# Performance work log

Measured on AMD Instinct MI355X. Metric: run time of the kernel, lower is better.

## Reference

```python
import jax, jax.numpy as jnp
import numpy as np
import math

B = 1024      # graphs
N = 64        # nodes per graph (padded, masked by node_mask)
BN = B * N    # total nodes
EPG = 192     # directed edges per graph
E = B * EPG


def setup_inputs() -> dict:
    key = jax.random.key(0)
    ks = jax.random.split(key, 40)

    def nrm(k, shp, s=0.02):
        return (jax.random.normal(k, shp) * s).astype(jnp.float32)

    mol_batch_x = jax.random.normal(ks[0], (BN, 19), dtype=jnp.float32)
    offs = jnp.arange(B, dtype=jnp.int32) * N
    src = jax.random.randint(ks[1], (B, EPG), 0, N, dtype=jnp.int32) + offs[:, None]
    dst = jax.random.randint(ks[2], (B, EPG), 0, N, dtype=jnp.int32) + offs[:, None]
    mol_batch_edge_index = jnp.stack([src.reshape(-1), dst.reshape(-1)], axis=0)
    mol_batch_batch = jnp.repeat(jnp.arange(B, dtype=jnp.int32), N)
    text_features = jax.random.normal(ks[3], (B, 300), dtype=jnp.float32)
    timesteps = jax.random.uniform(ks[4], (B,), minval=0.0, maxval=1000.0, dtype=jnp.float32)
    node_mask = (jax.random.uniform(ks[5], (B, N)) > 0.1).astype(jnp.float32)

    p = {
        'W_tr': nrm(ks[6], (19, 300)),   'b_tr': jnp.zeros((300,), jnp.float32),
        'W_c1': nrm(ks[7], (300, 600)),  'b_c1': jnp.zeros((600,), jnp.float32),
        'W_c2': nrm(ks[8], (600, 600)),  'b_c2': jnp.zeros((600,), jnp.float32),
        'W_c3': nrm(ks[9], (600, 600)),  'b_c3': jnp.zeros((600,), jnp.float32),
        'W_h1': nrm(ks[10], (600, 600)), 'b_h1': jnp.zeros((600,), jnp.float32),
        'W_h2': nrm(ks[11], (600, 600)), 'b_h2': jnp.zeros((600,), jnp.float32),
        'W_h3': nrm(ks[12], (600, 300)), 'b_h3': jnp.zeros((300,), jnp.float32),
        'ln_g': jnp.ones((300,), jnp.float32), 'ln_b': jnp.zeros((300,), jnp.float32),
        'W_t1': nrm(ks[13], (128, 512)), 'b_t1': jnp.zeros((512,), jnp.float32),
        'W_t2': nrm(ks[14], (512, 512)), 'b_t2': jnp.zeros((512,), jnp.float32),
        'W_e':  nrm(ks[15], (512, 3000)), 'b_e': jnp.zeros((3000,), jnp.float32),
    }
    return dict(mol_batch_x=mol_batch_x, mol_batch_edge_index=mol_batch_edge_index,
                mol_batch_batch=mol_batch_batch, text_features=text_features,
                timesteps=timesteps, node_mask=node_mask, **p)


def timestep_embedding(t, dim=128, max_period=10000.0):
    half = dim // 2
    freqs = jnp.exp(-math.log(max_period) * jnp.arange(half, dtype=jnp.float32) / half)
    args = t[:, None] * freqs[None]                 # [B, half]
    return jnp.concatenate([jnp.cos(args), jnp.sin(args)], axis=-1)  # [B, dim]


def gcn_conv(x, W, b, src, dst, num_nodes):
    # PyG GCNConv: D^{-1/2} (A + I) D^{-1/2} X W + b, edge weights 1
    h = x @ W                                             # [BN, F]
    deg = jnp.zeros((num_nodes,), h.dtype).at[dst].add(1.0) + 1.0  # in-degree + self-loop
    inv_sqrt = jax.lax.rsqrt(deg)
    coef = inv_sqrt[src] * inv_sqrt[dst]                  # [E]
    agg = jax.ops.segment_sum(h[src] * coef[:, None], dst, num_segments=num_nodes)
    return agg + h * (1.0 / deg)[:, None] + b             # self-loop norm = 1/deg


def global_mean_pool(x, batch, num_graphs):
    sums = jax.ops.segment_sum(x, batch, num_segments=num_graphs)
    cnts = jax.ops.segment_sum(jnp.ones((x.shape[0],), x.dtype), batch, num_segments=num_graphs)
    return sums / jnp.maximum(cnts, 1.0)[:, None]


def layer_norm(x, g, b, eps=1e-5):
    mu = jnp.mean(x, axis=-1, keepdims=True)
    var = jnp.mean(jnp.square(x - mu), axis=-1, keepdims=True)
    return (x - mu) * jax.lax.rsqrt(var + eps) * g + b


def reference(mol_batch_x, mol_batch_edge_index, mol_batch_batch, text_features,
              timesteps, node_mask, W_tr, b_tr, W_c1, b_c1, W_c2, b_c2, W_c3, b_c3,
              W_h1, b_h1, W_h2, b_h2, W_h3, b_h3, ln_g, ln_b,
              W_t1, b_t1, W_t2, b_t2, W_e, b_e):
    num_nodes = mol_batch_x.shape[0]
    num_graphs = node_mask.shape[0]
    src, dst = mol_batch_edge_index[0], mol_batch_edge_index[1]

    # FiLM conditioning from timestep embedding
    emb = jax.nn.relu(timestep_embedding(timesteps, 128) @ W_t1 + b_t1) @ W_t2 + b_t2  # [B,512]
    emb_out = jax.nn.relu(emb) @ W_e + b_e                                             # [B,3000]
    s1, t1 = emb_out[:, 0:600], emb_out[:, 600:1200]
    s2, t2 = emb_out[:, 1200:1800], emb_out[:, 1800:2400]
    s3, t3 = emb_out[:, 2400:2700], emb_out[:, 2700:3000]

    # node transform + mask
    x = mol_batch_x @ W_tr + b_tr                     # [BN, 300]
    x = x * node_mask.reshape(-1, 1)

    # GCN stack
    x = jax.nn.relu(gcn_conv(x, W_c1, b_c1, src, dst, num_nodes))
    x = jax.nn.relu(gcn_conv(x, W_c2, b_c2, src, dst, num_nodes))
    x = gcn_conv(x, W_c3, b_c3, src, dst, num_nodes)  # [BN, 600]

    g = global_mean_pool(x, mol_batch_batch, num_graphs)  # [B, 600]
    g = jax.nn.relu(g @ W_h1 + b_h1)
    g = g * (1.0 + s1) + t1
    g = jax.nn.relu(g @ W_h2 + b_h2)
    g = g * (1.0 + s2) + t2
    g = g @ W_h3 + b_h3                                # [B, 300]
    g = g * (1.0 + s3) + t3
    g = layer_norm(g, ln_g, ln_b)
    return (g, text_features)
```

## Files before the change

kernel.cpp:

```cpp
#include <hip/hip_runtime.h>
#include <hip/hip_bf16.h>
#include <cstdint>
#include <cstddef>

static constexpr int B   = 1024;
static constexpr int N   = 64;
static constexpr int BN  = B * N;
static constexpr int EPG = 192;
static constexpr int E   = B * EPG;
static constexpr int FP  = 608;
static constexpr int KP1 = 320;
static constexpr int PMS = 72;
static constexpr int NCONV = 2560;

typedef __hip_bfloat16 bf16;
typedef __bf16 bf16x8 __attribute__((ext_vector_type(8)));
typedef __bf16 bf16x4 __attribute__((ext_vector_type(4)));
typedef float  f32x4  __attribute__((ext_vector_type(4)));

__device__ __forceinline__ void storeC(float* p, float v) { *p = v; }
__device__ __forceinline__ void storeC(bf16* p, float v) { *p = __float2bfloat16(v); }

__device__ __forceinline__ void llds16(const void* g, void* l) {
    __builtin_amdgcn_global_load_lds(
        (const __attribute__((address_space(1))) unsigned int*)g,
        (__attribute__((address_space(3))) unsigned int*)l,
        16, 0, 0);
}


template<bool RELU, bool FILM, typename CT>
__device__ __forceinline__ void g64_tile(
    const bf16* __restrict__ A, int lda,
    const bf16* __restrict__ Bt, int ldb,
    const float* __restrict__ bias,
    CT* __restrict__ C, int ldc, int Ncap,
    const bf16* __restrict__ fS, const bf16* __restrict__ fT, int fstride,
    int K, int m0, int n0, char* lds, int tid)
{
    const int lane = tid & 63;
    const int w    = tid >> 6;
    const int wn   = w * 32;
    const int l15  = lane & 15;
    const int lhi  = lane >> 4;
    const int co   = (lhi ^ ((l15 >> 1) & 3)) << 3;
    const int nk   = K >> 5;

    auto stage = [&](int k0, char* buf) {
        {
            int row = tid >> 2;
            int kc  = (tid & 3) ^ ((row >> 1) & 3);
            llds16(A + (size_t)(m0 + row) * lda + k0 + kc * 8,
                   buf + (size_t)(w * 64) * 16);
        }
        #pragma unroll
        for (int t = 0; t < 2; ++t) {
            int ci  = t * 256 + tid;
            int row = ci >> 2;
            int kc  = (ci & 3) ^ ((row >> 1) & 3);
            llds16(Bt + (size_t)(n0 + row) * ldb + k0 + kc * 8,
                   buf + 4096 + (size_t)(t * 256 + w * 64) * 16);
        }
    };

    f32x4 acc[4][2] = {};
    stage(0, lds);
    asm volatile("s_waitcnt vmcnt(0)" ::: "memory");
    __syncthreads();

    for (int k = 0; k < nk; ++k) {
        if (k + 1 < nk) stage((k + 1) << 5, lds + ((k + 1) & 1) * 12288);

        __bf16* As = (__bf16*)(lds + (k & 1) * 12288);
        __bf16* Bs = As + 2048;
        bf16x8 af[4], bg[2];
        #pragma unroll
        for (int i = 0; i < 4; ++i)
            af[i] = *(bf16x8*)(As + (i * 16 + l15) * 32 + co);
        #pragma unroll
        for (int j = 0; j < 2; ++j)
            bg[j] = *(bf16x8*)(Bs + (wn + j * 16 + l15) * 32 + co);
        #pragma unroll
        for (int i = 0; i < 4; ++i)
            #pragma unroll
            for (int j = 0; j < 2; ++j)
                acc[i][j] = __builtin_amdgcn_mfma_f32_16x16x32_bf16(
                    af[i], bg[j], acc[i][j], 0, 0, 0);

        asm volatile("s_waitcnt vmcnt(0)" ::: "memory");
        __syncthreads();
    }

    #pragma unroll
    for (int i = 0; i < 4; ++i) {
        #pragma unroll
        for (int j = 0; j < 2; ++j) {
            int col = n0 + wn + j * 16 + l15;
            if (col < Ncap) {
                float bv = bias ? bias[col] : 0.f;
                #pragma unroll
                for (int e = 0; e < 4; ++e) {
                    int row = m0 + i * 16 + lhi * 4 + e;
                    float v = acc[i][j][e] + bv;
                    if (RELU) v = fmaxf(v, 0.f);
                    if (FILM) {
                        float sv = __bfloat162float(fS[(size_t)row * fstride + col]);
                        float tv = __bfloat162float(fT[(size_t)row * fstride + col]);
                        v = v * (1.f + sv) + tv;
                    }
                    storeC(&C[(size_t)row * ldc + col], v);
                }
            }
        }
    }
}

__device__ __attribute__((noinline)) void guest_g64(
    const bf16* gA, int glda, const bf16* gBt, int gldb,
    const float* gbias, bf16* gC, int gldc, int gNcap, int gK, int gnt,
    int t, char* lds, int tid)
{
    int mt2 = t / gnt, nt2 = t % gnt;
    g64_tile<true, false, bf16>(gA, glda, gBt, gldb, gbias, gC, gldc, gNcap,
                                nullptr, nullptr, 0, gK, mt2 * 64, nt2 * 128,
                                lds, tid);
}

template<bool RELU, bool FILM, typename CT>
__global__ __launch_bounds__(256) void gemm64(
    const bf16* __restrict__ A, int lda,
    const bf16* __restrict__ Bt, int ldb,
    const float* __restrict__ bias,
    CT* __restrict__ C, int ldc, int Ncap,
    const bf16* __restrict__ fS, const bf16* __restrict__ fT, int fstride,
    int K)
{
    __shared__ __align__(16) char lds[24576];
    g64_tile<RELU, FILM, CT>(A, lda, Bt, ldb, bias, C, ldc, Ncap,
                             fS, fT, fstride, K,
                             blockIdx.x * 64, blockIdx.y * 128, lds,
                             threadIdx.x);
}

__global__ __launch_bounds__(256) void k_two_gemms(
    const bf16* __restrict__ A2b, const bf16* __restrict__ Wet,
    const float* __restrict__ b_e, bf16* __restrict__ EO,
    const bf16* __restrict__ Yv, const bf16* __restrict__ Wb3,
    const float* __restrict__ b_c3, bf16* __restrict__ G0)
{
    __shared__ __align__(16) char lds[24576];
    int bid = blockIdx.x;
    if (bid < 384) {
        int mt = bid / 24, nt = bid % 24;
        g64_tile<false, false, bf16>(A2b, 512, Wet, 512, b_e, EO, 3000, 3000,
                                     nullptr, nullptr, 0, 512,
                                     mt * 64, nt * 128, lds, threadIdx.x);
    } else {
        int t = bid - 384;
        int mt = t / 5, nt = t % 5;
        g64_tile<false, false, bf16>(Yv, FP, Wb3, FP, b_c3, G0, FP, 600,
                                     nullptr, nullptr, 0, FP,
                                     mt * 64, nt * 128, lds, threadIdx.x);
    }
}

__global__ __launch_bounds__(256, 4) void conv1_gemm(
    const bf16* __restrict__ A,
    const bf16* __restrict__ Bt,
    const float* __restrict__ bias,
    bf16* __restrict__ X1,
    const bf16* __restrict__ gA, int glda,
    const bf16* __restrict__ gBt, int gldb,
    const float* __restrict__ gbias,
    bf16* __restrict__ gC, int gldc, int gNcap, int gK, int gnt)
{
    __shared__ __align__(16) char regA[32768];
    const int tid = threadIdx.x;
    const int bid = blockIdx.x;

    if (bid >= NCONV) {
        guest_g64(gA, glda, gBt, gldb, gbias, gC, gldc, gNcap, gK, gnt,
                  bid - NCONV, regA, tid);
        return;
    }

    const int lane = tid & 63;
    const int w    = tid >> 6;
    const int wm   = (w & 1) * 64;
    const int wn   = (w >> 1) * 64;
    const int l15  = lane & 15;
    const int lhi  = lane >> 4;
    const int co   = (lhi ^ ((l15 >> 1) & 3)) << 3;

    const int lid = bid >> 3;
    const int mt  = (bid & 7) * 64 + lid / 5;
    const int nt  = lid % 5;
    const int m0  = mt * 128;
    const int n0  = nt * 128;

    auto stage = [&](int k0, char* buf) {
        #pragma unroll
        for (int t = 0; t < 2; ++t) {
            int ci  = t * 256 + tid;
            int row = ci >> 2;
            int kc  = (ci & 3) ^ ((row >> 1) & 3);
            llds16(A  + (size_t)(m0 + row) * KP1 + k0 + kc * 8,
                   buf + (size_t)(t * 256 + w * 64) * 16);
            llds16(Bt + (size_t)(n0 + row) * KP1 + k0 + kc * 8,
                   buf + 8192 + (size_t)(t * 256 + w * 64) * 16);
        }
    };

    constexpr int nk = KP1 / 32;
    f32x4 acc[4][4] = {};
    stage(0, regA);
    asm volatile("s_waitcnt vmcnt(0)" ::: "memory");
    __syncthreads();

    for (int k = 0; k < nk; ++k) {
        if (k + 1 < nk) stage((k + 1) << 5, regA + ((k + 1) & 1) * 16384);

        __bf16* As = (__bf16*)(regA + (k & 1) * 16384);
        __bf16* Bs = As + 4096;
        bf16x8 af[4], bg[4];
        #pragma unroll
        for (int i = 0; i < 4; ++i)
            af[i] = *(bf16x8*)(As + (wm + i * 16 + l15) * 32 + co);
        #pragma unroll
        for (int j = 0; j < 4; ++j)
            bg[j] = *(bf16x8*)(Bs + (wn + j * 16 + l15) * 32 + co);
        #pragma unroll
        for (int i = 0; i < 4; ++i)
            #pragma unroll
            for (int j = 0; j < 4; ++j)
                acc[i][j] = __builtin_amdgcn_mfma_f32_16x16x32_bf16(
                    af[i], bg[j], acc[i][j], 0, 0, 0);

        asm volatile("s_waitcnt vmcnt(0)" ::: "memory");
        __syncthreads();
    }

    #pragma unroll
    for (int i = 0; i < 4; ++i)
        #pragma unroll
        for (int j = 0; j < 4; ++j) {
            int col = n0 + wn + j * 16 + l15;
            if (col < FP) {
                float bv = (col < 600) ? bias[col] : 0.f;
                #pragma unroll
                for (int e = 0; e < 4; ++e) {
                    int row = m0 + wm + i * 16 + lhi * 4 + e;
                    float v = fmaxf(acc[i][j][e] + bv, 0.f);
                    X1[(size_t)row * FP + col] = __float2bfloat16(v);
                }
            }
        }
}

__global__ __launch_bounds__(256, 4) void conv_fused_q(
    const bf16* __restrict__ A, int lda, int K,
    const bf16* __restrict__ Bt, int ldb,
    const bf16* __restrict__ Pmg,
    const float* __restrict__ bias,
    const float* __restrict__ qv,
    bf16* __restrict__ Y,
    const bf16* __restrict__ gA, int glda,
    const bf16* __restrict__ gBt, int gldb,
    const float* __restrict__ gbias,
    bf16* __restrict__ gC, int gldc, int gNcap, int gK, int gnt)
{
    __shared__ __align__(16) char regA[35840];
    __shared__ float s_q[128];

    const int tid = threadIdx.x;
    const int bid = blockIdx.x;

    if (bid >= NCONV) {
        guest_g64(gA, glda, gBt, gldb, gbias, gC, gldc, gNcap, gK, gnt,
                  bid - NCONV, regA, tid);
        return;
    }

    __bf16* Ts = (__bf16*)regA;
    __bf16* Pm = (__bf16*)(regA + 17408);

    const int lane = tid & 63;
    const int w    = tid >> 6;
    const int wm   = (w & 1) * 64;
    const int wn   = (w >> 1) * 64;
    const int l15  = lane & 15;
    const int lhi  = lane >> 4;
    const int co   = (lhi ^ ((l15 >> 1) & 3)) << 3;

    const int lid = bid >> 3;
    const int mt  = (bid & 7) * 64 + lid / 5;
    const int nt  = lid % 5;
    const int m0  = mt * 128;
    const int n0  = nt * 128;

    if (tid < 128) s_q[tid] = qv[mt * 128 + tid];

    auto stage = [&](int k0, char* buf) {
        #pragma unroll
        for (int t = 0; t < 2; ++t) {
            int ci  = t * 256 + tid;
            int row = ci >> 2;
            int kc  = (ci & 3) ^ ((row >> 1) & 3);
            llds16(A  + (size_t)(m0 + row) * lda + k0 + kc * 8,
                   buf + (size_t)(t * 256 + w * 64) * 16);
            llds16(Bt + (size_t)(n0 + row) * ldb + k0 + kc * 8,
                   buf + 8192 + (size_t)(t * 256 + w * 64) * 16);
        }
    };

    const int nk = K >> 5;
    f32x4 acc[4][4] = {};
    stage(0, regA);
    asm volatile("s_waitcnt vmcnt(0)" ::: "memory");
    __syncthreads();

    for (int k = 0; k < nk; ++k) {
        if (k + 1 < nk) {
            stage((k + 1) << 5, regA + ((k + 1) & 1) * 16384);
        } else {
            #pragma unroll
            for (int i = 0; i < 4; ++i)
                llds16(Pmg + (size_t)mt * (128 * PMS) + (size_t)(i * 256 + tid) * 8,
                       (char*)Pm + (size_t)(i * 256 + w * 64) * 16);
            if (w < 2)
                llds16(Pmg + (size_t)mt * (128 * PMS) + (size_t)(1024 + w * 64 + lane) * 8,
                       (char*)Pm + (size_t)(1024 + w * 64) * 16);
        }

        __bf16* As = (__bf16*)(regA + (k & 1) * 16384);
        __bf16* Bs = As + 4096;
        bf16x8 af[4], bg[4];
        #pragma unroll
        for (int i = 0; i < 4; ++i)
            af[i] = *(bf16x8*)(As + (wm + i * 16 + l15) * 32 + co);
        #pragma unroll
        for (int j = 0; j < 4; ++j)
            bg[j] = *(bf16x8*)(Bs + (wn + j * 16 + l15) * 32 + co);
        #pragma unroll
        for (int i = 0; i < 4; ++i)
            #pragma unroll
            for (int j = 0; j < 4; ++j)
                acc[i][j] = __builtin_amdgcn_mfma_f32_16x16x32_bf16(
                    af[i], bg[j], acc[i][j], 0, 0, 0);

        asm volatile("s_waitcnt vmcnt(0)" ::: "memory");
        __syncthreads();
    }

    const int g  = w & 1;
    const int nb = w >> 1;
    #pragma unroll
    for (int h = 0; h < 2; ++h) {
        if (wn == h * 64) {
            #pragma unroll
            for (int i = 0; i < 4; ++i)
                #pragma unroll
                for (int j = 0; j < 4; ++j) {
                    int c_local = j * 16 + l15;
                    int rbase   = wm + i * 16 + lhi * 4;
                    bf16x4 pk;
                    #pragma unroll
                    for (int e = 0; e < 4; ++e) pk[e] = (__bf16)acc[i][j][e];
                    *(bf16x4*)(Ts + c_local * 136 + rbase) = pk;
                }
        }
        __syncthreads();

        f32x4 acc2[4][2] = {};
        #pragma unroll
        for (int k0 = 0; k0 < 64; k0 += 32) {
            bf16x8 pa[4], hb[2];
            #pragma unroll
            for (int i = 0; i < 4; ++i)
                pa[i] = *(bf16x8*)(Pm + (g * 64 + i * 16 + l15) * PMS + k0 + lhi * 8);
            #pragma unroll
            for (int j = 0; j < 2; ++j)
                hb[j] = *(bf16x8*)(Ts + (nb * 32 + j * 16 + l15) * 136
                                      + g * 64 + k0 + lhi * 8);
            #pragma unroll
            for (int i = 0; i < 4; ++i)
                #pragma unroll
                for (int j = 0; j < 2; ++j)
                    acc2[i][j] = __builtin_amdgcn_mfma_f32_16x16x32_bf16(
                        pa[i], hb[j], acc2[i][j], 0, 0, 0);
        }
        #pragma unroll
        for (int j = 0; j < 2; ++j) {
            int col = n0 + h * 64 + nb * 32 + j * 16 + l15;
            float bv = (col < 600) ? bias[col] : 0.f;
            float yp = 0.f;
            #pragma unroll
            for (int i = 0; i < 4; ++i)
                #pragma unroll
                for (int e = 0; e < 4; ++e) {
                    float v = fmaxf(acc2[i][j][e] + bv, 0.f);
                    yp += s_q[g * 64 + i * 16 + lhi * 4 + e] * v;
                }
            yp += __shfl_xor(yp, 16, 64);
            yp += __shfl_xor(yp, 32, 64);
            if (lhi == 0 && col < FP)
                Y[(size_t)(mt * 2 + g) * FP + col] = __float2bfloat16(yp);
        }
        __syncthreads();
    }
}

struct WtJob  { const float* src; bf16* dst; int Ksrc, Nsrc, Kp, Np, blk0; };
struct PrepArgs {
    WtJob j[9];
    int nwt, te0, pp0, xtr0;
    const int*   ei;
    const float* ts;
    const float* xin; const float* Wtr; const float* btr; const float* mask;
    bf16* TE; bf16* Pmg; float* qv; bf16* PX0;
};

__global__ __launch_bounds__(256) void k_prep(PrepArgs a)
{
    __shared__ __align__(16) char sm[35840];
    const int bx  = blockIdx.x;
    const int tid = threadIdx.x;

    if (bx < a.nwt) {
        int ji = 0;
        while (ji < 8 && bx >= a.j[ji + 1].blk0) ++ji;
        WtJob jb = a.j[ji];
        int t  = bx - jb.blk0;
        int kt = (jb.Kp + 63) >> 6;
        int ti = t % kt, tj = t / kt;
        int kg0 = ti * 64, ng0 = tj * 64;
        float (*T)[65] = (float(*)[65])sm;
        #pragma unroll 4
        for (int r = 0; r < 16; ++r) {
            int kl = (tid >> 6) + r * 4, nl = tid & 63;
            int kg = kg0 + kl, ng = ng0 + nl;
// ... 100 lines not shown
        __syncthreads();
        for (int idx = tid; idx < 64 * 20; idx += 256) {
            int r = idx / 20, j = idx - r * 20;
            float s = 0.f;
            #pragma unroll 8
            for (int s2 = 0; s2 < 64; ++s2)
                s += Pf[r * 64 + s2] * xm[s2 * 20 + j];
            xa[idx] = s;
        }
        __syncthreads();
        for (int idx = tid; idx < 19 * 304; idx += 256) {
            int k = idx / 304, c = idx - k * 304;
            Ws[idx] = (c < 300) ? a.Wtr[k * 300 + c] : 0.f;
        }
        for (int c = tid; c < 304; c += 256)
            sb[c] = (c < 300) ? a.btr[c] : 0.f;
        __syncthreads();
        int n  = tid >> 2;
        int c0 = tid & 3;
        float ba = xa[n * 20 + 19];
        for (int c = c0; c < 304; c += 4) {
            float acc = ba * sb[c];
            #pragma unroll
            for (int k = 0; k < 19; ++k)
                acc += xa[n * 20 + k] * Ws[k * 304 + c];
            a.PX0[(size_t)(g * 64 + n) * KP1 + c] = __float2bfloat16(acc);
        }
        bf16x8 z = {};
        for (int idx = tid; idx < 64 * 2; idx += 256) {
            int nn = idx >> 1, jv = idx & 1;
            *(bf16x8*)((__bf16*)a.PX0 + (size_t)(g * 64 + nn) * KP1 + 304 + jv * 8) = z;
        }
    }
}

__global__ __launch_bounds__(256) void k_ln_copy(const float* __restrict__ G,
                                                 const float* __restrict__ lg,
                                                 const float* __restrict__ lb,
                                                 const float* __restrict__ text,
                                                 float* __restrict__ out)
{
    int r = blockIdx.x;
    int tid = threadIdx.x;
    __shared__ float red[4];
    __shared__ float smu, svar;

    float v0 = (tid < 300) ? G[r * 300 + tid] : 0.f;
    float v1 = (tid + 256 < 300) ? G[r * 300 + tid + 256] : 0.f;
    float s = v0 + v1;
    #pragma unroll
    for (int o = 32; o > 0; o >>= 1) s += __shfl_down(s, o, 64);
    if ((tid & 63) == 0) red[tid >> 6] = s;
    __syncthreads();
    if (tid == 0) smu = (red[0] + red[1] + red[2] + red[3]) * (1.f / 300.f);
    __syncthreads();
    float mu = smu;
    float d0 = (tid < 300) ? v0 - mu : 0.f;
    float d1 = (tid + 256 < 300) ? v1 - mu : 0.f;
    s = d0 * d0 + d1 * d1;
    #pragma unroll
    for (int o = 32; o > 0; o >>= 1) s += __shfl_down(s, o, 64);
    if ((tid & 63) == 0) red[tid >> 6] = s;
    __syncthreads();
    if (tid == 0) svar = (red[0] + red[1] + red[2] + red[3]) * (1.f / 300.f);
    __syncthreads();
    float rstd = rsqrtf(svar + 1e-5f);
    if (tid < 300)
        out[r * 300 + tid] = d0 * rstd * lg[tid] + lb[tid];
    if (tid + 256 < 300)
        out[r * 300 + tid + 256] = d1 * rstd * lg[tid + 256] + lb[tid + 256];
    float* o2 = out + (size_t)B * 300;
    for (int c = tid; c < 300; c += 256)
        o2[(size_t)r * 300 + c] = text[(size_t)r * 300 + c];
}

extern "C" void kernel_launch(void* const* d_in, const int* in_sizes, int n_in,
                              void* d_out, int out_size, void* d_ws, size_t ws_size,
                              hipStream_t stream)
{
    const float* x_in  = (const float*)d_in[0];
    const int*   ei    = (const int*)d_in[1];
    const float* text  = (const float*)d_in[3];
    const float* tst   = (const float*)d_in[4];
    const float* mask  = (const float*)d_in[5];
    const float* W_tr  = (const float*)d_in[6];
    const float* b_tr  = (const float*)d_in[7];
    const float* W_c1  = (const float*)d_in[8];
    const float* b_c1  = (const float*)d_in[9];
    const float* W_c2  = (const float*)d_in[10];
    const float* b_c2  = (const float*)d_in[11];
    const float* W_c3  = (const float*)d_in[12];
    const float* b_c3  = (const float*)d_in[13];
    const float* W_h1  = (const float*)d_in[14];
    const float* b_h1  = (const float*)d_in[15];
    const float* W_h2  = (const float*)d_in[16];
    const float* b_h2  = (const float*)d_in[17];
    const float* W_h3  = (const float*)d_in[18];
    const float* b_h3  = (const float*)d_in[19];
    const float* ln_g  = (const float*)d_in[20];
    const float* ln_b  = (const float*)d_in[21];
    const float* W_t1  = (const float*)d_in[22];
    const float* b_t1  = (const float*)d_in[23];
    const float* W_t2  = (const float*)d_in[24];
    const float* b_t2  = (const float*)d_in[25];
    const float* W_e   = (const float*)d_in[26];
    const float* b_e   = (const float*)d_in[27];
// ... 29 lines not shown
    float* qv     = (float*)carve((size_t)BN * 4);
    (void)ws_size; (void)in_sizes; (void)n_in; (void)out_size;

    float* out = (float*)d_out;

    PrepArgs pa;
    struct JD { const float* s; bf16* d; int Ks, Ns, Kp, Np; };
    JD jd[9] = {
        { W_c1, Wb1,  300, 600,  KP1, 640 },
        { W_c2, Wb2,  600, 600,  FP,  640 },
        { W_c3, Wb3,  600, 600,  FP,  640 },
        { W_t1, Wt1t, 128, 512,  128, 512 },
        { W_t2, Wt2t, 512, 512,  512, 512 },
        { W_e,  Wet,  512, 3000, 512, 3072 },
        { W_h1, Wh1t, 600, 600,  FP,  640 },
        { W_h2, Wh2t, 600, 600,  FP,  640 },
        { W_h3, Wh3t, 600, 300,  FP,  384 },
    };
    int cum = 0;
    for (int i = 0; i < 9; ++i) {
        int kt = (jd[i].Kp + 63) >> 6, nt = (jd[i].Np + 63) >> 6;
        pa.j[i] = { jd[i].s, jd[i].d, jd[i].Ks, jd[i].Ns, jd[i].Kp, jd[i].Np, cum };
        cum += kt * nt;
    }
    pa.nwt  = cum;
    pa.te0  = cum;       cum += (B * 128) / 256;
    pa.pp0  = cum;       cum += B / 2;
    pa.xtr0 = cum;       cum += B;
    pa.ei = ei; pa.ts = tst;
    pa.xin = x_in; pa.Wtr = W_tr; pa.btr = b_tr; pa.mask = mask;
    pa.TE = TE; pa.Pmg = Pmg; pa.qv = qv; pa.PX0 = PX0;
    k_prep<<<cum, 256, 0, stream>>>(pa);

    conv1_gemm<<<NCONV + 64, 256, 0, stream>>>(
        PX0, Wb1, b_c1, X1,
        TE, 128, Wt1t, 128, b_t1, A1b, 512, 512, 128, 4);

    conv_fused_q<<<NCONV + 64, 256, 0, stream>>>(
        X1, FP, FP, Wb2, FP, Pmg, b_c2, qv, Yv,
        A1b, 512, Wt2t, 512, b_t2, A2b, 512, 512, 512, 4);

    k_two_gemms<<<464, 256, 0, stream>>>(A2b, Wet, b_e, EO, Yv, Wb3, b_c3, G0);

    gemm64<true, true, bf16><<<dim3(16, 5), 256, 0, stream>>>(
        G0, FP, Wh1t, FP, b_h1, G1, FP, 600, EO + 0, EO + 600, 3000, FP);
    gemm64<true, true, bf16><<<dim3(16, 5), 256, 0, stream>>>(
        G1, FP, Wh2t, FP, b_h2, G2, FP, 600, EO + 1200, EO + 1800, 3000, FP);
    gemm64<false, true, float><<<dim3(16, 3), 256, 0, stream>>>(
        G2, FP, Wh3t, FP, b_h3, G3, 300, 300, EO + 2400, EO + 2700, 3000, FP);

    k_ln_copy<<<B, 256, 0, stream>>>(G3, ln_g, ln_b, text, out);
}
```

Before: 341.5 us.

## Load B operands directly to registers and triple-buffer A in LDS

Reworks the GEMM mainloops (g64_tile, conv1_gemm, conv_fused_q) so that B fragments go straight from global memory into registers instead of being staged in LDS. A now runs through a three-slot LDS ring with prefetch distance two, and the loop waits with partial vmcnt counts and a single barrier rather than a full drain and two syncs per step. The Pm prefetch in conv_fused_q moves before the loop, and LDS sizes and launch bounds are retuned. The aim is less LDS traffic and fewer stalls. The risks are uncoalesced per-lane global B loads, fragile hand-counted vmcnt values, and higher register pressure.

```diff
diff --git a/kernel.cpp b/kernel.cpp
--- a/kernel.cpp
+++ b/kernel.cpp
@@ -28,6 +28,12 @@
         16, 0, 0);
 }
 
+__device__ __forceinline__ void pipe_barrier() {
+    __builtin_amdgcn_s_barrier();
+    asm volatile("" ::: "memory");
+}
+#define FENCE() asm volatile("" ::: "memory")
+
 
 template<bool RELU, bool FILM, typename CT>
 __device__ __forceinline__ void g64_tile(
@@ -46,49 +52,47 @@
     const int co   = (lhi ^ ((l15 >> 1) & 3)) << 3;
     const int nk   = K >> 5;
 
-    auto stage = [&](int k0, char* buf) {
-        {
-            int row = tid >> 2;
-            int kc  = (tid & 3) ^ ((row >> 1) & 3);
-            llds16(A + (size_t)(m0 + row) * lda + k0 + kc * 8,
-                   buf + (size_t)(w * 64) * 16);
-        }
-        #pragma unroll
-        for (int t = 0; t < 2; ++t) {
-            int ci  = t * 256 + tid;
-            int row = ci >> 2;
-            int kc  = (ci & 3) ^ ((row >> 1) & 3);
-            llds16(Bt + (size_t)(n0 + row) * ldb + k0 + kc * 8,
-                   buf + 4096 + (size_t)(t * 256 + w * 64) * 16);
-        }
-    };
+    const int arow = tid >> 2;
+    const int akc  = (tid & 3) ^ ((arow >> 1) & 3);
+    const bf16* aS = A + (size_t)(m0 + arow) * lda + akc * 8;
+    const size_t aOff = (size_t)(w * 64) * 16;
+
+    const bf16* bS0 = Bt + (size_t)(n0 + wn + l15) * ldb + lhi * 8;
+    const bf16* bS1 = bS0 + (size_t)16 * ldb;
+
+    bf16x8 bg0, bg1;
+    llds16(aS, lds + aOff);
+    FENCE();
+    bg0 = *(const bf16x8*)(bS0);
+    bg1 = *(const bf16x8*)(bS1);
+    FENCE();
+    llds16(aS + 32, lds + 4096 + aOff);
 
     f32x4 acc[4][2] = {};
-    stage(0, lds);
-    asm volatile("s_waitcnt vmcnt(0)" ::: "memory");
-    __syncthreads();
-
+    int cur = 0;
     for (int k = 0; k < nk; ++k) {
-        if (k + 1 < nk) stage((k + 1) << 5, lds + ((k + 1) & 1) * 12288);
-
-        __bf16* As = (__bf16*)(lds + (k & 1) * 12288);
-        __bf16* Bs = As + 2048;
-        bf16x8 af[4], bg[2];
+        if (k == nk - 1) asm volatile("s_waitcnt vmcnt(2)" ::: "memory");
+        else             asm volatile("s_waitcnt vmcnt(3)" ::: "memory");
+        pipe_barrier();
+        if (k + 2 < nk) {
+            int nb3 = cur ? cur - 1 : 2;
+            llds16(aS + ((k + 2) << 5), lds + nb3 * 4096 + aOff);
+        }
+        __bf16* As = (__bf16*)(lds + cur * 4096);
+        bf16x8 af[4];
         #pragma unroll
         for (int i = 0; i < 4; ++i)
             af[i] = *(bf16x8*)(As + (i * 16 + l15) * 32 + co);
         #pragma unroll
-        for (int j = 0; j < 2; ++j)
-            bg[j] = *(bf16x8*)(Bs + (wn + j * 16 + l15) * 32 + co);
-        #pragma unroll
-        for (int i = 0; i < 4; ++i)
-            #pragma unroll
-            for (int j = 0; j < 2; ++j)
-                acc[i][j] = __builtin_amdgcn_mfma_f32_16x16x32_bf16(
-                    af[i], bg[j], acc[i][j], 0, 0, 0);
-
-        asm volatile("s_waitcnt vmcnt(0)" ::: "memory");
-        __syncthreads();
+        for (int i = 0; i < 4; ++i) {
+            acc[i][0] = __builtin_amdgcn_mfma_f32_16x16x32_bf16(af[i], bg0, acc[i][0], 0, 0, 0);
+            acc[i][1] = __builtin_amdgcn_mfma_f32_16x16x32_bf16(af[i], bg1, acc[i][1], 0, 0, 0);
+        }
+        if (k + 1 < nk) {
+            bg0 = *(const bf16x8*)(bS0 + ((k + 1) << 5));
+            bg1 = *(const bf16x8*)(bS1 + ((k + 1) << 5));
+        }
+        cur = (cur == 2) ? 0 : cur + 1;
     }
 
     #pragma unroll
@@ -127,7 +131,7 @@
 }
 
 template<bool RELU, bool FILM, typename CT>
-__global__ __launch_bounds__(256) void gemm64(
+__global__ __launch_bounds__(256, 4) void gemm64(
     const bf16* __restrict__ A, int lda,
     const bf16* __restrict__ Bt, int ldb,
     const float* __restrict__ bias,
@@ -135,20 +139,20 @@
     const bf16* __restrict__ fS, const bf16* __restrict__ fT, int fstride,
     int K)
 {
-    __shared__ __align__(16) char lds[24576];
+    __shared__ __align__(16) char lds[12288];
     g64_tile<RELU, FILM, CT>(A, lda, Bt, ldb, bias, C, ldc, Ncap,
                              fS, fT, fstride, K,
                              blockIdx.x * 64, blockIdx.y * 128, lds,
                              threadIdx.x);
 }
 
-__global__ __launch_bounds__(256) void k_two_gemms(
+__global__ __launch_bounds__(256, 4) void k_two_gemms(
     const bf16* __restrict__ A2b, const bf16* __restrict__ Wet,
     const float* __restrict__ b_e, bf16* __restrict__ EO,
     const bf16* __restrict__ Yv, const bf16* __restrict__ Wb3,
     const float* __restrict__ b_c3, bf16* __restrict__ G0)
 {
-    __shared__ __align__(16) char lds[24576];
+    __shared__ __align__(16) char lds[12288];
     int bid = blockIdx.x;
     if (bid < 384) {
         int mt = bid / 24, nt = bid % 24;
@@ -174,7 +178,7 @@
     const float* __restrict__ gbias,
     bf16* __restrict__ gC, int gldc, int gNcap, int gK, int gnt)
 {
-    __shared__ __align__(16) char regA[32768];
+    __shared__ __align__(16) char regA[24576];
     const int tid = threadIdx.x;
     const int bid = blockIdx.x;
 
@@ -198,46 +202,52 @@
     const int m0  = mt * 128;
     const int n0  = nt * 128;
 
-    auto stage = [&](int k0, char* buf) {
+    auto stageA = [&](int k0, char* buf) {
         #pragma unroll
         for (int t = 0; t < 2; ++t) {
             int ci  = t * 256 + tid;
             int row = ci >> 2;
             int kc  = (ci & 3) ^ ((row >> 1) & 3);
-            llds16(A  + (size_t)(m0 + row) * KP1 + k0 + kc * 8,
+            llds16(A + (size_t)(m0 + row) * KP1 + k0 + kc * 8,
                    buf + (size_t)(t * 256 + w * 64) * 16);
-            llds16(Bt + (size_t)(n0 + row) * KP1 + k0 + kc * 8,
-                   buf + 8192 + (size_t)(t * 256 + w * 64) * 16);
         }
     };
+    const bf16* bB = Bt + (size_t)(n0 + wn + l15) * KP1 + lhi * 8;
+    bf16x8 bg[4];
+    auto loadB = [&](int k0) {
+        #pragma unroll
+        for (int j = 0; j < 4; ++j)
+            bg[j] = *(const bf16x8*)(bB + (size_t)j * 16 * KP1 + k0);
+    };
 
     constexpr int nk = KP1 / 32;
+    stageA(0, regA);
+    FENCE();
+    loadB(0);
+    FENCE();
+    stageA(32, regA + 8192);
+
     f32x4 acc[4][4] = {};
-    stage(0, regA);
-    asm volatile("s_waitcnt vmcnt(0)" ::: "memory");
-    __syncthreads();
-
+    int cur = 0;
     for (int k = 0; k < nk; ++k) {
-        if (k + 1 < nk) stage((k + 1) << 5, regA + ((k + 1) & 1) * 16384);
-
-        __bf16* As = (__bf16*)(regA + (k & 1) * 16384);
-        __bf16* Bs = As + 4096;
-        bf16x8 af[4], bg[4];
+        if (k == nk - 1) asm volatile("s_waitcnt vmcnt(4)" ::: "memory");
+        else             asm volatile("s_waitcnt vmcnt(6)" ::: "memory");
+        pipe_barrier();
+        if (k + 2 < nk) stageA((k + 2) << 5, regA + (cur ? cur - 1 : 2) * 8192);
+
+        __bf16* As = (__bf16*)(regA + cur * 8192);
+        bf16x8 af[4];
         #pragma unroll
         for (int i = 0; i < 4; ++i)
             af[i] = *(bf16x8*)(As + (wm + i * 16 + l15) * 32 + co);
-        #pragma unroll
-        for (int j = 0; j < 4; ++j)
-            bg[j] = *(bf16x8*)(Bs + (wn + j * 16 + l15) * 32 + co);
         #pragma unroll
         for (int i = 0; i < 4; ++i)
             #pragma unroll
             for (int j = 0; j < 4; ++j)
                 acc[i][j] = __builtin_amdgcn_mfma_f32_16x16x32_bf16(
                     af[i], bg[j], acc[i][j], 0, 0, 0);
-
-        asm volatile("s_waitcnt vmcnt(0)" ::: "memory");
-        __syncthreads();
+        if (k + 1 < nk) loadB((k + 1) << 5);
+        cur = (cur == 2) ? 0 : cur + 1;
     }
 
     #pragma unroll
@@ -257,7 +267,7 @@
         }
 }
 
-__global__ __launch_bounds__(256, 4) void conv_fused_q(
+__global__ __launch_bounds__(256, 3) void conv_fused_q(
     const bf16* __restrict__ A, int lda, int K,
     const bf16* __restrict__ Bt, int ldb,
     const bf16* __restrict__ Pmg,
@@ -269,7 +279,7 @@
     const float* __restrict__ gbias,
     bf16* __restrict__ gC, int gldc, int gNcap, int gK, int gnt)
 {
-    __shared__ __align__(16) char regA[35840];
+    __shared__ __align__(16) char regA[43008];
     __shared__ float s_q[128];
 
     const int tid = threadIdx.x;
@@ -282,7 +292,7 @@
     }
 
     __bf16* Ts = (__bf16*)regA;
-    __bf16* Pm = (__bf16*)(regA + 17408);
+    __bf16* Pm = (__bf16*)(regA + 24576);
 
     const int lane = tid & 63;
     const int w    = tid >> 6;
@@ -300,57 +310,63 @@
 
     if (tid < 128) s_q[tid] = qv[mt * 128 + tid];
 
-    auto stage = [&](int k0, char* buf) {
+    #pragma unroll
+    for (int i = 0; i < 4; ++i)
+        llds16(Pmg + (size_t)mt * (128 * PMS) + (size_t)(i * 256 + tid) * 8,
+               (char*)Pm + (size_t)(i * 256 + w * 64) * 16);
+    if (w < 2)
+        llds16(Pmg + (size_t)mt * (128 * PMS) + (size_t)(1024 + w * 64 + lane) * 8,
+               (char*)Pm + (size_t)(1024 + w * 64) * 16);
+    FENCE();
+
+    auto stageA = [&](int k0, char* buf) {
         #pragma unroll
         for (int t = 0; t < 2; ++t) {
             int ci  = t * 256 + tid;
             int row = ci >> 2;
             int kc  = (ci & 3) ^ ((row >> 1) & 3);
-            llds16(A  + (size_t)(m0 + row) * lda + k0 + kc * 8,
+            llds16(A + (size_t)(m0 + row) * lda + k0 + kc * 8,
                    buf + (size_t)(t * 256 + w * 64) * 16);
-            llds16(Bt + (size_t)(n0 + row) * ldb + k0 + kc * 8,
-                   buf + 8192 + (size_t)(t * 256 + w * 64) * 16);
         }
     };
+    const bf16* bB = Bt + (size_t)(n0 + wn + l15) * ldb + lhi * 8;
+    bf16x8 bg[4];
+    auto loadB = [&](int k0) {
+        #pragma unroll
+        for (int j = 0; j < 4; ++j)
+            bg[j] = *(const bf16x8*)(bB + (size_t)j * 16 * ldb + k0);
+    };
 
     const int nk = K >> 5;
+    stageA(0, regA);
+    FENCE();
+    loadB(0);
+    FENCE();
+    stageA(32, regA + 8192);
+
     f32x4 acc[4][4] = {};
-    stage(0, regA);
-    asm volatile("s_waitcnt vmcnt(0)" ::: "memory");
-    __syncthreads();
-
+    int cur = 0;
     for (int k = 0; k < nk; ++k) {
-        if (k + 1 < nk) {
-            stage((k + 1) << 5, regA + ((k + 1) & 1) * 16384);
-        } else {
-            #pragma unroll
-            for (int i = 0; i < 4; ++i)
-                llds16(Pmg + (size_t)mt * (128 * PMS) + (size_t)(i * 256 + tid) * 8,
-                       (char*)Pm + (size_t)(i * 256 + w * 64) * 16);
-            if (w < 2)
-                llds16(Pmg + (size_t)mt * (128 * PMS) + (size_t)(1024 + w * 64 + lane) * 8,
-                       (char*)Pm + (size_t)(1024 + w * 64) * 16);
-        }
-
-        __bf16* As = (__bf16*)(regA + (k & 1) * 16384);
-        __bf16* Bs = As + 4096;
-        bf16x8 af[4], bg[4];
+        if (k == nk - 1) asm volatile("s_waitcnt vmcnt(4)" ::: "memory");
+        else             asm volatile("s_waitcnt vmcnt(6)" ::: "memory");
+        pipe_barrier();
+        if (k + 2 < nk) stageA((k + 2) << 5, regA + (cur ? cur - 1 : 2) * 8192);
+
+        __bf16* As = (__bf16*)(regA + cur * 8192);
+        bf16x8 af[4];
         #pragma unroll
         for (int i = 0; i < 4; ++i)
             af[i] = *(bf16x8*)(As + (wm + i * 16 + l15) * 32 + co);
-        #pragma unroll
-        for (int j = 0; j < 4; ++j)
-            bg[j] = *(bf16x8*)(Bs + (wn + j * 16 + l15) * 32 + co);
         #pragma unroll
         for (int i = 0; i < 4; ++i)
             #pragma unroll
             for (int j = 0; j < 4; ++j)
                 acc[i][j] = __builtin_amdgcn_mfma_f32_16x16x32_bf16(
                     af[i], bg[j], acc[i][j], 0, 0, 0);
-
-        asm volatile("s_waitcnt vmcnt(0)" ::: "memory");
-        __syncthreads();
-    }
+        if (k + 1 < nk) loadB((k + 1) << 5);
+        cur = (cur == 2) ? 0 : cur + 1;
+    }
+    __syncthreads();
 
     const int g  = w & 1;
     const int nb = w >> 1;
```

Measured after the change: 382.8 us. 12.1% more time.

## Fuse tail GEMMs and layernorm into one cooperative kernel with grid syncs

Applied to the files above, without the earlier changes.

The five small tail launches (the emb/conv3 GEMM pair, three FiLM head GEMMs and the layernorm/copy) are merged into a single cooperative kernel of 464 blocks. Grid-wide syncs separate the stages, and the layernorm rows are strided across blocks. This removes per-launch overhead and idle gaps between tiny kernels. In exchange, most blocks sit idle during the 80- and 48-tile stages and the grid barriers add their own cost.

```diff
diff --git a/kernel.cpp b/kernel.cpp
--- a/kernel.cpp
+++ b/kernel.cpp
@@ -1,7 +1,10 @@
 #include <hip/hip_runtime.h>
 #include <hip/hip_bf16.h>
+#include <hip/hip_cooperative_groups.h>
 #include <cstdint>
 #include <cstddef>
+
+namespace cg = cooperative_groups;
 
 static constexpr int B   = 1024;
 static constexpr int N   = 64;
@@ -126,44 +129,6 @@
                                 lds, tid);
 }
 
-template<bool RELU, bool FILM, typename CT>
-__global__ __launch_bounds__(256) void gemm64(
-    const bf16* __restrict__ A, int lda,
-    const bf16* __restrict__ Bt, int ldb,
-    const float* __restrict__ bias,
-    CT* __restrict__ C, int ldc, int Ncap,
-    const bf16* __restrict__ fS, const bf16* __restrict__ fT, int fstride,
-    int K)
-{
-    __shared__ __align__(16) char lds[24576];
-    g64_tile<RELU, FILM, CT>(A, lda, Bt, ldb, bias, C, ldc, Ncap,
-                             fS, fT, fstride, K,
-                             blockIdx.x * 64, blockIdx.y * 128, lds,
-                             threadIdx.x);
-}
-
-__global__ __launch_bounds__(256) void k_two_gemms(
-    const bf16* __restrict__ A2b, const bf16* __restrict__ Wet,
-    const float* __restrict__ b_e, bf16* __restrict__ EO,
-    const bf16* __restrict__ Yv, const bf16* __restrict__ Wb3,
-    const float* __restrict__ b_c3, bf16* __restrict__ G0)
-{
-    __shared__ __align__(16) char lds[24576];
-    int bid = blockIdx.x;
-    if (bid < 384) {
-        int mt = bid / 24, nt = bid % 24;
-        g64_tile<false, false, bf16>(A2b, 512, Wet, 512, b_e, EO, 3000, 3000,
-                                     nullptr, nullptr, 0, 512,
-                                     mt * 64, nt * 128, lds, threadIdx.x);
-    } else {
-        int t = bid - 384;
-        int mt = t / 5, nt = t % 5;
-        g64_tile<false, false, bf16>(Yv, FP, Wb3, FP, b_c3, G0, FP, 600,
-                                     nullptr, nullptr, 0, FP,
-                                     mt * 64, nt * 128, lds, threadIdx.x);
-    }
-}
-
 __global__ __launch_bounds__(256, 4) void conv1_gemm(
     const bf16* __restrict__ A,
     const bf16* __restrict__ Bt,
@@ -406,6 +371,98 @@
             if (lhi == 0 && col < FP)
                 Y[(size_t)(mt * 2 + g) * FP + col] = __float2bfloat16(yp);
         }
+        __syncthreads();
+    }
+}
+
+struct TailArgs {
+    const bf16* A2b; const bf16* Wet; const float* b_e; bf16* EO;
+    const bf16* Yv;  const bf16* Wb3; const float* b_c3; bf16* G0;
+    const bf16* Wh1t; const float* b_h1; bf16* G1;
+    const bf16* Wh2t; const float* b_h2; bf16* G2;
+    const bf16* Wh3t; const float* b_h3; float* G3;
+    const float* ln_g; const float* ln_b; const float* text; float* out;
+};
+
+__global__ __launch_bounds__(256) void k_tail(TailArgs a)
+{
+    __shared__ __align__(16) char lds[24576];
+    const int bid = blockIdx.x;
+    const int tid = threadIdx.x;
+    cg::grid_group grid = cg::this_grid();
+
+    if (bid < 384) {
+        int mt = bid / 24, nt = bid % 24;
+        g64_tile<false, false, bf16>(a.A2b, 512, a.Wet, 512, a.b_e, a.EO, 3000,
+                                     3000, nullptr, nullptr, 0, 512,
+                                     mt * 64, nt * 128, lds, tid);
+    } else {
+        int t = bid - 384;
+        int mt = t / 5, nt = t % 5;
+        g64_tile<false, false, bf16>(a.Yv, FP, a.Wb3, FP, a.b_c3, a.G0, FP, 600,
+                                     nullptr, nullptr, 0, FP,
+                                     mt * 64, nt * 128, lds, tid);
+    }
+    __threadfence();
+    grid.sync();
+
+    if (bid < 80) {
+        int mt = bid / 5, nt = bid % 5;
+        g64_tile<true, true, bf16>(a.G0, FP, a.Wh1t, FP, a.b_h1, a.G1, FP, 600,
+                                   a.EO + 0, a.EO + 600, 3000, FP,
+                                   mt * 64, nt * 128, lds, tid);
+    }
+    __threadfence();
+    grid.sync();
+
+    if (bid < 80) {
+        int mt = bid / 5, nt = bid % 5;
+        g64_tile<true, true, bf16>(a.G1, FP, a.Wh2t, FP, a.b_h2, a.G2, FP, 600,
+                                   a.EO + 1200, a.EO + 1800, 3000, FP,
+                                   mt * 64, nt * 128, lds, tid);
+    }
+    __threadfence();
+    grid.sync();
+
+    if (bid < 48) {
+        int mt = bid / 3, nt = bid % 3;
+        g64_tile<false, true, float>(a.G2, FP, a.Wh3t, FP, a.b_h3, a.G3, 300,
+                                     300, a.EO + 2400, a.EO + 2700, 3000, FP,
+                                     mt * 64, nt * 128, lds, tid);
+    }
+    __threadfence();
+    grid.sync();
+
+    float* red = (float*)lds;
+    float* svv = (float*)lds + 8;
+    for (int r = bid; r < B; r += (int)gridDim.x) {
+        float v0 = (tid < 300) ? a.G3[r * 300 + tid] : 0.f;
+        float v1 = (tid + 256 < 300) ? a.G3[r * 300 + tid + 256] : 0.f;
+        float s = v0 + v1;
+        #pragma unroll
+        for (int o = 32; o > 0; o >>= 1) s += __shfl_down(s, o, 64);
+        if ((tid & 63) == 0) red[tid >> 6] = s;
+        __syncthreads();
+        if (tid == 0) svv[0] = (red[0] + red[1] + red[2] + red[3]) * (1.f / 300.f);
+        __syncthreads();
+        float mu = svv[0];
+        float d0 = (tid < 300) ? v0 - mu : 0.f;
+        float d1 = (tid + 256 < 300) ? v1 - mu : 0.f;
+        s = d0 * d0 + d1 * d1;
+        #pragma unroll
+        for (int o = 32; o > 0; o >>= 1) s += __shfl_down(s, o, 64);
+        if ((tid & 63) == 0) red[tid >> 6] = s;
+        __syncthreads();
+        if (tid == 0) svv[1] = (red[0] + red[1] + red[2] + red[3]) * (1.f / 300.f);
+        __syncthreads();
+        float rstd = rsqrtf(svv[1] + 1e-5f);
+        if (tid < 300)
+            a.out[r * 300 + tid] = d0 * rstd * a.ln_g[tid] + a.ln_b[tid];
+        if (tid + 256 < 300)
+            a.out[r * 300 + tid + 256] = d1 * rstd * a.ln_g[tid + 256] + a.ln_b[tid + 256];
+        float* o2 = a.out + (size_t)B * 300;
+        for (int c = tid; c < 300; c += 256)
+            o2[(size_t)r * 300 + c] = a.text[(size_t)r * 300 + c];
         __syncthreads();
     }
 }
@@ -572,46 +629,6 @@
             *(bf16x8*)((__bf16*)a.PX0 + (size_t)(g * 64 + nn) * KP1 + 304 + jv * 8) = z;
         }
     }
-}
-
-__global__ __launch_bounds__(256) void k_ln_copy(const float* __restrict__ G,
-                                                 const float* __restrict__ lg,
-                                                 const float* __restrict__ lb,
-                                                 const float* __restrict__ text,
-                                                 float* __restrict__ out)
-{
-    int r = blockIdx.x;
-    int tid = threadIdx.x;
-    __shared__ float red[4];
-    __shared__ float smu, svar;
-
-    float v0 = (tid < 300) ? G[r * 300 + tid] : 0.f;
-    float v1 = (tid + 256 < 300) ? G[r * 300 + tid + 256] : 0.f;
-    float s = v0 + v1;
-    #pragma unroll
-    for (int o = 32; o > 0; o >>= 1) s += __shfl_down(s, o, 64);
-    if ((tid & 63) == 0) red[tid >> 6] = s;
-    __syncthreads();
-    if (tid == 0) smu = (red[0] + red[1] + red[2] + red[3]) * (1.f / 300.f);
-    __syncthreads();
-    float mu = smu;
-    float d0 = (tid < 300) ? v0 - mu : 0.f;
-    float d1 = (tid + 256 < 300) ? v1 - mu : 0.f;
-    s = d0 * d0 + d1 * d1;
-    #pragma unroll
-    for (int o = 32; o > 0; o >>= 1) s += __shfl_down(s, o, 64);
-    if ((tid & 63) == 0) red[tid >> 6] = s;
-    __syncthreads();
-    if (tid == 0) svar = (red[0] + red[1] + red[2] + red[3]) * (1.f / 300.f);
-    __syncthreads();
-    float rstd = rsqrtf(svar + 1e-5f);
-    if (tid < 300)
-        out[r * 300 + tid] = d0 * rstd * lg[tid] + lb[tid];
-    if (tid + 256 < 300)
-        out[r * 300 + tid + 256] = d1 * rstd * lg[tid + 256] + lb[tid + 256];
-    float* o2 = out + (size_t)B * 300;
-    for (int c = tid; c < 300; c += 256)
-        o2[(size_t)r * 300 + c] = text[(size_t)r * 300 + c];
 }
 
 extern "C" void kernel_launch(void* const* d_in, const int* in_sizes, int n_in,
@@ -715,14 +732,14 @@
         X1, FP, FP, Wb2, FP, Pmg, b_c2, qv, Yv,
         A1b, 512, Wt2t, 512, b_t2, A2b, 512, 512, 512, 4);
 
-    k_two_gemms<<<464, 256, 0, stream>>>(A2b, Wet, b_e, EO, Yv, Wb3, b_c3, G0);
-
-    gemm64<true, true, bf16><<<dim3(16, 5), 256, 0, stream>>>(
-        G0, FP, Wh1t, FP, b_h1, G1, FP, 600, EO + 0, EO + 600, 3000, FP);
-    gemm64<true, true, bf16><<<dim3(16, 5), 256, 0, stream>>>(
-        G1, FP, Wh2t, FP, b_h2, G2, FP, 600, EO + 1200, EO + 1800, 3000, FP);
-    gemm64<false, true, float><<<dim3(16, 3), 256, 0, stream>>>(
-        G2, FP, Wh3t, FP, b_h3, G3, 300, 300, EO + 2400, EO + 2700, 3000, FP);
-
-    k_ln_copy<<<B, 256, 0, stream>>>(G3, ln_g, ln_b, text, out);
+    TailArgs ta;
+    ta.A2b = A2b;  ta.Wet = Wet;   ta.b_e = b_e;   ta.EO = EO;
+    ta.Yv = Yv;    ta.Wb3 = Wb3;   ta.b_c3 = b_c3; ta.G0 = G0;
+    ta.Wh1t = Wh1t; ta.b_h1 = b_h1; ta.G1 = G1;
+    ta.Wh2t = Wh2t; ta.b_h2 = b_h2; ta.G2 = G2;
+    ta.Wh3t = Wh3t; ta.b_h3 = b_h3; ta.G3 = G3;
+    ta.ln_g = ln_g; ta.ln_b = ln_b; ta.text = text; ta.out = out;
+    void* targs[] = { &ta };
+    hipLaunchCooperativeKernel((const void*)k_tail, dim3(464), dim3(256),
+                               targs, 0, stream);
 }
```

Measured after the change: 767.5 us. 2.25x slower.

## Double conv kernel block size to 512 threads with halved per-wave tiles

Applied to the files above, without the earlier changes.

The two GCN conv GEMM kernels now launch 512 threads per block instead of 256. The same 128x128 block tile is split across 8 waves, so each wave owns a 64x32 sub-tile with half the accumulators. Staging, the second-stage aggregation GEMM and the guest GEMM tile (a new 8-wave variant) are rewritten to match. The aim is more waves in flight for latency hiding and lower register pressure per wave, at the cost of more LDS fragment reads per MFMA and more barrier participants.

```diff
diff --git a/kernel.cpp b/kernel.cpp
--- a/kernel.cpp
+++ b/kernel.cpp
@@ -115,15 +115,81 @@
     }
 }
 
+__device__ __forceinline__ void g64_tile8(
+    const bf16* __restrict__ A, int lda,
+    const bf16* __restrict__ Bt, int ldb,
+    const float* __restrict__ bias,
+    bf16* __restrict__ C, int ldc, int Ncap,
+    int K, int m0, int n0, char* lds, int tid)
+{
+    const int lane = tid & 63;
+    const int w    = tid >> 6;
+    const int wn   = w * 16;
+    const int l15  = lane & 15;
+    const int lhi  = lane >> 4;
+    const int co   = (lhi ^ ((l15 >> 1) & 3)) << 3;
+    const int nk   = K >> 5;
+
+    auto stage = [&](int k0, char* buf) {
+        if (tid < 256) {
+            int row = tid >> 2;
+            int kc  = (tid & 3) ^ ((row >> 1) & 3);
+            llds16(A + (size_t)(m0 + row) * lda + k0 + kc * 8,
+                   buf + (size_t)(w * 64) * 16);
+        }
+        {
+            int row = tid >> 2;
+            int kc  = (tid & 3) ^ ((row >> 1) & 3);
+            llds16(Bt + (size_t)(n0 + row) * ldb + k0 + kc * 8,
+                   buf + 4096 + (size_t)(w * 64) * 16);
+        }
+    };
+
+    f32x4 acc[4] = {};
+    stage(0, lds);
+    asm volatile("s_waitcnt vmcnt(0)" ::: "memory");
+    __syncthreads();
+
+    for (int k = 0; k < nk; ++k) {
+        if (k + 1 < nk) stage((k + 1) << 5, lds + ((k + 1) & 1) * 12288);
+
+        __bf16* As = (__bf16*)(lds + (k & 1) * 12288);
+        __bf16* Bs = As + 2048;
+        bf16x8 af[4], bg;
+        #pragma unroll
+        for (int i = 0; i < 4; ++i)
+            af[i] = *(bf16x8*)(As + (i * 16 + l15) * 32 + co);
+        bg = *(bf16x8*)(Bs + (wn + l15) * 32 + co);
+        #pragma unroll
+        for (int i = 0; i < 4; ++i)
+            acc[i] = __builtin_amdgcn_mfma_f32_16x16x32_bf16(af[i], bg, acc[i], 0, 0, 0);
+
+        asm volatile("s_waitcnt vmcnt(0)" ::: "memory");
+        __syncthreads();
+    }
+
+    int col = n0 + wn + l15;
+    if (col < Ncap) {
+        float bv = bias ? bias[col] : 0.f;
+        #pragma unroll
+        for (int i = 0; i < 4; ++i)
+            #pragma unroll
+            for (int e = 0; e < 4; ++e) {
+                int row = m0 + i * 16 + lhi * 4 + e;
+                float v = fmaxf(acc[i][e] + bv, 0.f);
+                C[(size_t)row * ldc + col] = __float2bfloat16(v);
+            }
+    }
+}
+
 __device__ __attribute__((noinline)) void guest_g64(
     const bf16* gA, int glda, const bf16* gBt, int gldb,
     const float* gbias, bf16* gC, int gldc, int gNcap, int gK, int gnt,
     int t, char* lds, int tid)
 {
     int mt2 = t / gnt, nt2 = t % gnt;
-    g64_tile<true, false, bf16>(gA, glda, gBt, gldb, gbias, gC, gldc, gNcap,
-                                nullptr, nullptr, 0, gK, mt2 * 64, nt2 * 128,
-                                lds, tid);
+    g64_tile8(gA, glda, gBt, gldb, gbias, gC, gldc, gNcap,
+              gK, mt2 * 64, nt2 * 128, lds, tid);
 }
 
 template<bool RELU, bool FILM, typename CT>
@@ -164,7 +230,7 @@
     }
 }
 
-__global__ __launch_bounds__(256, 4) void conv1_gemm(
+__global__ __launch_bounds__(512, 6) void conv1_gemm(
     const bf16* __restrict__ A,
     const bf16* __restrict__ Bt,
     const float* __restrict__ bias,
@@ -187,7 +253,7 @@
     const int lane = tid & 63;
     const int w    = tid >> 6;
     const int wm   = (w & 1) * 64;
-    const int wn   = (w >> 1) * 64;
+    const int wn   = (w >> 1) * 32;
     const int l15  = lane & 15;
     const int lhi  = lane >> 4;
     const int co   = (lhi ^ ((l15 >> 1) & 3)) << 3;
@@ -199,20 +265,16 @@
     const int n0  = nt * 128;
 
     auto stage = [&](int k0, char* buf) {
-        #pragma unroll
-        for (int t = 0; t < 2; ++t) {
-            int ci  = t * 256 + tid;
-            int row = ci >> 2;
-            int kc  = (ci & 3) ^ ((row >> 1) & 3);
-            llds16(A  + (size_t)(m0 + row) * KP1 + k0 + kc * 8,
-                   buf + (size_t)(t * 256 + w * 64) * 16);
-            llds16(Bt + (size_t)(n0 + row) * KP1 + k0 + kc * 8,
-                   buf + 8192 + (size_t)(t * 256 + w * 64) * 16);
-        }
+        int row = tid >> 2;
+        int kc  = (tid & 3) ^ ((row >> 1) & 3);
+        llds16(A  + (size_t)(m0 + row) * KP1 + k0 + kc * 8,
+               buf + (size_t)(w * 64) * 16);
+        llds16(Bt + (size_t)(n0 + row) * KP1 + k0 + kc * 8,
+               buf + 8192 + (size_t)(w * 64) * 16);
     };
 
     constexpr int nk = KP1 / 32;
-    f32x4 acc[4][4] = {};
+    f32x4 acc[4][2] = {};
     stage(0, regA);
     asm volatile("s_waitcnt vmcnt(0)" ::: "memory");
     __syncthreads();
@@ -222,17 +284,17 @@
 
         __bf16* As = (__bf16*)(regA + (k & 1) * 16384);
         __bf16* Bs = As + 4096;
-        bf16x8 af[4], bg[4];
+        bf16x8 af[4], bg[2];
         #pragma unroll
         for (int i = 0; i < 4; ++i)
             af[i] = *(bf16x8*)(As + (wm + i * 16 + l15) * 32 + co);
         #pragma unroll
-        for (int j = 0; j < 4; ++j)
+        for (int j = 0; j < 2; ++j)
             bg[j] = *(bf16x8*)(Bs + (wn + j * 16 + l15) * 32 + co);
         #pragma unroll
         for (int i = 0; i < 4; ++i)
             #pragma unroll
-            for (int j = 0; j < 4; ++j)
+            for (int j = 0; j < 2; ++j)
                 acc[i][j] = __builtin_amdgcn_mfma_f32_16x16x32_bf16(
                     af[i], bg[j], acc[i][j], 0, 0, 0);
 
@@ -243,7 +305,7 @@
     #pragma unroll
     for (int i = 0; i < 4; ++i)
         #pragma unroll
-        for (int j = 0; j < 4; ++j) {
+        for (int j = 0; j < 2; ++j) {
             int col = n0 + wn + j * 16 + l15;
             if (col < FP) {
                 float bv = (col < 600) ? bias[col] : 0.f;
@@ -257,7 +319,7 @@
         }
 }
 
-__global__ __launch_bounds__(256, 4) void conv_fused_q(
+__global__ __launch_bounds__(512, 6) void conv_fused_q(
     const bf16* __restrict__ A, int lda, int K,
     const bf16* __restrict__ Bt, int ldb,
     const bf16* __restrict__ Pmg,
@@ -287,7 +349,7 @@
     const int lane = tid & 63;
     const int w    = tid >> 6;
     const int wm   = (w & 1) * 64;
-    const int wn   = (w >> 1) * 64;
+    const int wn   = (w >> 1) * 32;
     const int l15  = lane & 15;
     const int lhi  = lane >> 4;
     const int co   = (lhi ^ ((l15 >> 1) & 3)) << 3;
@@ -301,20 +363,16 @@
     if (tid < 128) s_q[tid] = qv[mt * 128 + tid];
 
     auto stage = [&](int k0, char* buf) {
-        #pragma unroll
-        for (int t = 0; t < 2; ++t) {
-            int ci  = t * 256 + tid;
-            int row = ci >> 2;
-            int kc  = (ci & 3) ^ ((row >> 1) & 3);
-            llds16(A  + (size_t)(m0 + row) * lda + k0 + kc * 8,
-                   buf + (size_t)(t * 256 + w * 64) * 16);
-            llds16(Bt + (size_t)(n0 + row) * ldb + k0 + kc * 8,
-                   buf + 8192 + (size_t)(t * 256 + w * 64) * 16);
-        }
+        int row = tid >> 2;
+        int kc  = (tid & 3) ^ ((row >> 1) & 3);
+        llds16(A  + (size_t)(m0 + row) * lda + k0 + kc * 8,
+               buf + (size_t)(w * 64) * 16);
+        llds16(Bt + (size_t)(n0 + row) * ldb + k0 + kc * 8,
+               buf + 8192 + (size_t)(w * 64) * 16);
     };
 
     const int nk = K >> 5;
-    f32x4 acc[4][4] = {};
+    f32x4 acc[4][2] = {};
     stage(0, regA);
     asm volatile("s_waitcnt vmcnt(0)" ::: "memory");
     __syncthreads();
@@ -324,9 +382,9 @@
             stage((k + 1) << 5, regA + ((k + 1) & 1) * 16384);
         } else {
             #pragma unroll
-            for (int i = 0; i < 4; ++i)
-                llds16(Pmg + (size_t)mt * (128 * PMS) + (size_t)(i * 256 + tid) * 8,
-                       (char*)Pm + (size_t)(i * 256 + w * 64) * 16);
+            for (int i = 0; i < 2; ++i)
+                llds16(Pmg + (size_t)mt * (128 * PMS) + (size_t)(i * 512 + tid) * 8,
+                       (char*)Pm + (size_t)(i * 512 + w * 64) * 16);
             if (w < 2)
                 llds16(Pmg + (size_t)mt * (128 * PMS) + (size_t)(1024 + w * 64 + lane) * 8,
                        (char*)Pm + (size_t)(1024 + w * 64) * 16);
@@ -334,17 +392,17 @@
 
         __bf16* As = (__bf16*)(regA + (k & 1) * 16384);
         __bf16* Bs = As + 4096;
-        bf16x8 af[4], bg[4];
+        bf16x8 af[4], bg[2];
         #pragma unroll
         for (int i = 0; i < 4; ++i)
             af[i] = *(bf16x8*)(As + (wm + i * 16 + l15) * 32 + co);
         #pragma unroll
-        for (int j = 0; j < 4; ++j)
+        for (int j = 0; j < 2; ++j)
             bg[j] = *(bf16x8*)(Bs + (wn + j * 16 + l15) * 32 + co);
         #pragma unroll
         for (int i = 0; i < 4; ++i)
             #pragma unroll
-            for (int j = 0; j < 4; ++j)
+            for (int j = 0; j < 2; ++j)
                 acc[i][j] = __builtin_amdgcn_mfma_f32_16x16x32_bf16(
                     af[i], bg[j], acc[i][j], 0, 0, 0);
 
@@ -356,12 +414,12 @@
     const int nb = w >> 1;
     #pragma unroll
     for (int h = 0; h < 2; ++h) {
-        if (wn == h * 64) {
+        if ((w >> 2) == h) {
             #pragma unroll
             for (int i = 0; i < 4; ++i)
                 #pragma unroll
-                for (int j = 0; j < 4; ++j) {
-                    int c_local = j * 16 + l15;
+                for (int j = 0; j < 2; ++j) {
+                    int c_local = (wn & 63) + j * 16 + l15;
                     int rbase   = wm + i * 16 + lhi * 4;
                     bf16x4 pk;
                     #pragma unroll
@@ -371,34 +429,28 @@
         }
         __syncthreads();
 
-        f32x4 acc2[4][2] = {};
+        f32x4 acc2[4] = {};
         #pragma unroll
         for (int k0 = 0; k0 < 64; k0 += 32) {
-            bf16x8 pa[4], hb[2];
+            bf16x8 pa[4], hb;
             #pragma unroll
             for (int i = 0; i < 4; ++i)
                 pa[i] = *(bf16x8*)(Pm + (g * 64 + i * 16 + l15) * PMS + k0 + lhi * 8);
-            #pragma unroll
-            for (int j = 0; j < 2; ++j)
-                hb[j] = *(bf16x8*)(Ts + (nb * 32 + j * 16 + l15) * 136
-                                      + g * 64 + k0 + lhi * 8);
+            hb = *(bf16x8*)(Ts + (nb * 16 + l15) * 136 + g * 64 + k0 + lhi * 8);
             #pragma unroll
             for (int i = 0; i < 4; ++i)
-                #pragma unroll
-                for (int j = 0; j < 2; ++j)
-                    acc2[i][j] = __builtin_amdgcn_mfma_f32_16x16x32_bf16(
-                        pa[i], hb[j], acc2[i][j], 0, 0, 0);
-        }
-        #pragma unroll
-        for (int j = 0; j < 2; ++j) {
-            int col = n0 + h * 64 + nb * 32 + j * 16 + l15;
+                acc2[i] = __builtin_amdgcn_mfma_f32_16x16x32_bf16(
+                    pa[i], hb, acc2[i], 0, 0, 0);
+        }
+        {
+            int col = n0 + h * 64 + nb * 16 + l15;
             float bv = (col < 600) ? bias[col] : 0.f;
             float yp = 0.f;
             #pragma unroll
             for (int i = 0; i < 4; ++i)
                 #pragma unroll
                 for (int e = 0; e < 4; ++e) {
-                    float v = fmaxf(acc2[i][j][e] + bv, 0.f);
+                    float v = fmaxf(acc2[i][e] + bv, 0.f);
                     yp += s_q[g * 64 + i * 16 + lhi * 4 + e] * v;
                 }
             yp += __shfl_xor(yp, 16, 64);
@@ -707,11 +759,11 @@
     pa.TE = TE; pa.Pmg = Pmg; pa.qv = qv; pa.PX0 = PX0;
     k_prep<<<cum, 256, 0, stream>>>(pa);
 
-    conv1_gemm<<<NCONV + 64, 256, 0, stream>>>(
+    conv1_gemm<<<NCONV + 64, 512, 0, stream>>>(
         PX0, Wb1, b_c1, X1,
         TE, 128, Wt1t, 128, b_t1, A1b, 512, 512, 128, 4);
 
-    conv_fused_q<<<NCONV + 64, 256, 0, stream>>>(
+    conv_fused_q<<<NCONV + 64, 512, 0, stream>>>(
         X1, FP, FP, Wb2, FP, Pmg, b_c2, qv, Yv,
         A1b, 512, Wt2t, 512, b_t2, A2b, 512, 512, 512, 4);
 
```

Result: no change. 342.4 us (+0.3%).
